# Kernel tuning notes

Measured on AMD Instinct MI355X. Metric: run time of the kernel, lower is better.

The kernel has to match this reference:

```python
import jax, jax.numpy as jnp
import numpy as np

N, C, H, W = 8, 192, 112, 112
TEMPERATURE = 0.1


def setup_inputs() -> dict:
    key = jax.random.key(0)
    k1, k2 = jax.random.split(key)
    features = jax.random.normal(k1, (N, C, H, W), dtype=jnp.float32)
    # Raw per-pixel directions in {-1, 0, 1}; clip the neighbor coordinate into
    # bounds and recompute the direction so EVERY neighbor is valid. The torch
    # module's broadcasting (labels[:, i, j] vs an (N, M) gather) only works when
    # all N neighbors are valid at each pixel, so this matches its assumptions.
    raw = jax.random.randint(k2, (N, 2, H, W), -1, 2)
    ii = jnp.arange(H)[None, :, None]
    jj = jnp.arange(W)[None, None, :]
    d0 = jnp.clip(ii + raw[:, 0], 0, H - 1) - ii
    d1 = jnp.clip(jj + raw[:, 1], 0, W - 1) - jj
    directions = jnp.stack([d0, d1], axis=1).astype(jnp.int32)
    # Single-class labels: the original loss is -inf whenever any mask entry is 0
    # (log of exactly 0), so a finite, comparable baseline needs matching labels.
    labels = jnp.zeros((N, H, W), dtype=jnp.int32)
    return {"features": features, "labels": labels, "directions": directions}


def reference(features, labels, directions):
    # F.normalize(features, dim=1): x / max(||x||_2, eps)
    norm = jnp.linalg.norm(features, axis=1, keepdims=True)
    fn = features / jnp.maximum(norm, 1e-12)

    ii = jnp.arange(H)[None, :, None]
    jj = jnp.arange(W)[None, None, :]
    ni = ii + directions[:, 0]  # (N, H, W), in-bounds by construction
    nj = jj + directions[:, 1]  # (N, H, W)

    # Torch: features[:, :, neighbor_i, neighbor_j] gathers the M(==N) neighbor
    # coordinates across ALL batch elements -> (N, C, N, H, W) = [n, c, m, i, j]
    gathered = fn[:, :, ni, nj]
    # logits[n, m, i, j] = <fn[n, :, i, j], fn[n, :, ni[m,i,j], nj[m,i,j]]> / T
    logits = jnp.einsum('ncij,ncmij->nmij', fn, gathered) / TEMPERATURE

    # mask[n, m, i, j] = (labels[m, i, j] == labels[n, ni[m,i,j], nj[m,i,j]])
    # (torch broadcasts labels[:, i, j] along the first axis of the (N, M) gather)
    labels_g = labels[:, ni, nj]  # (N, N, H, W) = [n, m, i, j]
    mask = (labels[None, :, :, :] == labels_g).astype(fn.dtype)

    exp_l = jnp.exp(logits) * mask
    denom = jnp.sum(exp_l, axis=1, keepdims=True)  # sum over m
    # sum_{i,j} mean_{n,m}(.) / (H*W) == global mean over (n, m, i, j)
    loss = (-jnp.log(exp_l / (denom + 1e-6))).mean()
    return loss
```

## Files before the change

kernel.cpp:

```cpp
#include <hip/hip_runtime.h>
#include <math.h>


namespace {
constexpr int N_ = 8, C_ = 192, H_ = 112, W_ = 112;
constexpr int HW = H_ * W_;
constexpr int TPY = 8, TPX = 16;
constexpr int RS = 19;
constexpr int SLOTE = 192;
constexpr int NT = 128;
constexpr int CW = C_ / 2;
constexpr int KCH = 8;
constexpr int GRP = KCH / 2;
constexpr int NCHUNK = CW / KCH;
constexpr int GX = W_ / TPX, GY = H_ / TPY;
constexpr int NBLK = GX * GY * N_;
constexpr float INV_T = 10.0f;
constexpr double TOTAL = (double)N_ * N_ * H_ * W_;
}

__device__ __forceinline__ float sel3(int d, float a, float b, float c) {
    float r = (d < 0) ? a : b;
    return (d > 0) ? c : r;
}

__device__ __forceinline__ float px_loss(
    const float l[3][3], int gi, int gj, int n,
    const int* __restrict__ labels, const int* __restrict__ dirs)
{
    const int pix = gi * W_ + gj;
    float denom = 0.f, sumlog = 0.f;
#pragma unroll
    for (int m = 0; m < N_; ++m) {
        int d0 = dirs[((m * 2 + 0) * H_ + gi) * W_ + gj];
        int d1 = dirs[((m * 2 + 1) * H_ + gi) * W_ + gj];
        float r0 = sel3(d1, l[0][0], l[0][1], l[0][2]);
        float r1 = sel3(d1, l[1][0], l[1][1], l[1][2]);
        float r2 = sel3(d1, l[2][0], l[2][1], l[2][2]);
        float lm = sel3(d0, r0, r1, r2);
        int labm = labels[m * HW + pix];
        int labn = labels[n * HW + (gi + d0) * W_ + (gj + d1)];
        bool msk = (labm == labn);
        float e = msk ? __expf(lm) : 0.f;
        denom += e;
        sumlog += msk ? lm : -INFINITY;
    }
    return 8.0f * __logf(denom + 1e-6f) - sumlog;
}

extern "C" __global__ void __launch_bounds__(NT, 2)
dcl_main(const float* __restrict__ feat,
         const int* __restrict__ labels,
         const int* __restrict__ dirs,
         double* __restrict__ partial, int use_partial)
{
    __shared__ float2 tl[2 * 2 * GRP * SLOTE];
    __shared__ float  ssb[SLOTE];
    __shared__ float2 exch[64 * 9];

    const int tid = threadIdx.x, lane = tid & 63, wv = tid >> 6;
    const int gx0 = blockIdx.x * TPX, gy0 = blockIdx.y * TPY, n = blockIdx.z;

    int g0, g1, g2;
    {
        int s = lane, r = s / RS, c = s - r * RS;
        g0 = min(max(gy0 + r - 1, 0), H_ - 1) * W_ + min(max(gx0 + c - 1, 0), W_ - 1);
        s = lane + 64; r = s / RS; c = s - r * RS;
        g1 = min(max(gy0 + r - 1, 0), H_ - 1) * W_ + min(max(gx0 + c - 1, 0), W_ - 1);
        s = lane + 128; r = s / RS; c = s - r * RS;
        g2 = min(max(gy0 + r - 1, 0), H_ - 1) * W_ + min(max(gx0 + c - 1, 0), W_ - 1);
    }
    const int py = lane >> 3, pxp = lane & 7;
    const int wb = py * RS + 2 * pxp;
    const float* __restrict__ plane =
        feat + ((size_t)n * C_ + (size_t)wv * CW) * HW;

#define TLP(buf, g) (tl + (((wv * 2 + (buf)) * GRP + (g)) * SLOTE))

    float sA[9], sB[9];
    #pragma unroll
    for (int k = 0; k < 9; ++k) { sA[k] = 0.f; sB[k] = 0.f; }
    float ss0 = 0.f, ss1 = 0.f, ss2 = 0.f;

    {
        float v[24];
        #pragma unroll
        for (int k = 0; k < KCH; ++k) {
            v[k]      = plane[(size_t)k * HW + g0];
            v[8 + k]  = plane[(size_t)k * HW + g1];
            v[16 + k] = plane[(size_t)k * HW + g2];
        }
        #pragma unroll
        for (int g = 0; g < GRP; ++g) {
            TLP(0, g)[lane]       = make_float2(v[2 * g],      v[2 * g + 1]);
            TLP(0, g)[lane + 64]  = make_float2(v[8 + 2 * g],  v[8 + 2 * g + 1]);
            TLP(0, g)[lane + 128] = make_float2(v[16 + 2 * g], v[16 + 2 * g + 1]);
        }
        #pragma unroll
        for (int k = 0; k < KCH; ++k) {
            ss0 = fmaf(v[k], v[k], ss0);
            ss1 = fmaf(v[8 + k], v[8 + k], ss1);
            ss2 = fmaf(v[16 + k], v[16 + k], ss2);
        }
    }

    for (int t = 0; t < NCHUNK; ++t) {
        float v[24];
        const bool more = (t + 1 < NCHUNK);
        if (more) {
            const float* p = plane + (size_t)(t + 1) * KCH * HW;
            #pragma unroll
            for (int k = 0; k < KCH; ++k) {
                v[k]      = p[(size_t)k * HW + g0];
                v[8 + k]  = p[(size_t)k * HW + g1];
                v[16 + k] = p[(size_t)k * HW + g2];
            }
        }
        const int buf = t & 1;
        #pragma unroll
        for (int g = 0; g < GRP; ++g) {
            const float2* __restrict__ cp = TLP(buf, g);
            float2 w00 = cp[wb],          w01 = cp[wb + 1],          w02 = cp[wb + 2],          w03 = cp[wb + 3];
            float2 w10 = cp[wb + RS],     w11 = cp[wb + RS + 1],     w12 = cp[wb + RS + 2],     w13 = cp[wb + RS + 3];
            float2 w20 = cp[wb + 2 * RS], w21 = cp[wb + 2 * RS + 1], w22 = cp[wb + 2 * RS + 2], w23 = cp[wb + 2 * RS + 3];
            const float2 fA = w11, fB = w12;
            sA[0] = fmaf(fA.x, w00.x, fmaf(fA.y, w00.y, sA[0]));
            sA[1] = fmaf(fA.x, w01.x, fmaf(fA.y, w01.y, sA[1]));
            sA[2] = fmaf(fA.x, w02.x, fmaf(fA.y, w02.y, sA[2]));
            sA[3] = fmaf(fA.x, w10.x, fmaf(fA.y, w10.y, sA[3]));
            sA[4] = fmaf(fA.x, w11.x, fmaf(fA.y, w11.y, sA[4]));
            sA[5] = fmaf(fA.x, w12.x, fmaf(fA.y, w12.y, sA[5]));
            sA[6] = fmaf(fA.x, w20.x, fmaf(fA.y, w20.y, sA[6]));
            sA[7] = fmaf(fA.x, w21.x, fmaf(fA.y, w21.y, sA[7]));
            sA[8] = fmaf(fA.x, w22.x, fmaf(fA.y, w22.y, sA[8]));
            sB[0] = fmaf(fB.x, w01.x, fmaf(fB.y, w01.y, sB[0]));
            sB[1] = fmaf(fB.x, w02.x, fmaf(fB.y, w02.y, sB[1]));
            sB[2] = fmaf(fB.x, w03.x, fmaf(fB.y, w03.y, sB[2]));
            sB[3] = fmaf(fB.x, w11.x, fmaf(fB.y, w11.y, sB[3]));
            sB[4] = fmaf(fB.x, w12.x, fmaf(fB.y, w12.y, sB[4]));
            sB[5] = fmaf(fB.x, w13.x, fmaf(fB.y, w13.y, sB[5]));
            sB[6] = fmaf(fB.x, w21.x, fmaf(fB.y, w21.y, sB[6]));
            sB[7] = fmaf(fB.x, w22.x, fmaf(fB.y, w22.y, sB[7]));
            sB[8] = fmaf(fB.x, w23.x, fmaf(fB.y, w23.y, sB[8]));
        }
        if (more) {
            const int nb = buf ^ 1;
            #pragma unroll
            for (int g = 0; g < GRP; ++g) {
                TLP(nb, g)[lane]       = make_float2(v[2 * g],      v[2 * g + 1]);
                TLP(nb, g)[lane + 64]  = make_float2(v[8 + 2 * g],  v[8 + 2 * g + 1]);
                TLP(nb, g)[lane + 128] = make_float2(v[16 + 2 * g], v[16 + 2 * g + 1]);
            }
            #pragma unroll
            for (int k = 0; k < KCH; ++k) {
                ss0 = fmaf(v[k], v[k], ss0);
                ss1 = fmaf(v[8 + k], v[8 + k], ss1);
                ss2 = fmaf(v[16 + k], v[16 + k], ss2);
            }
        }
    }

    if (wv == 1) {
        #pragma unroll
        for (int k = 0; k < 9; ++k) exch[lane * 9 + k] = make_float2(sA[k], sB[k]);
        ssb[lane] = ss0; ssb[lane + 64] = ss1; ssb[lane + 128] = ss2;
    }
    __syncthreads();
    if (wv == 0) {
        ssb[lane]       = 1.0f / fmaxf(sqrtf(ss0 + ssb[lane]), 1e-12f);
        ssb[lane + 64]  = 1.0f / fmaxf(sqrtf(ss1 + ssb[lane + 64]), 1e-12f);
        ssb[lane + 128] = 1.0f / fmaxf(sqrtf(ss2 + ssb[lane + 128]), 1e-12f);
    }
    __syncthreads();

    if (wv == 0) {
        #pragma unroll
        for (int k = 0; k < 9; ++k) {
            float2 e = exch[lane * 9 + k];
            sA[k] += e.x; sB[k] += e.y;
        }
        float iv[3][4];
        #pragma unroll
        for (int r = 0; r < 3; ++r)
            #pragma unroll
            for (int c = 0; c < 4; ++c)
                iv[r][c] = ssb[wb + r * RS + c];
        const float iA = iv[1][1] * INV_T, iB = iv[1][2] * INV_T;
        float lA[3][3], lB[3][3];
        #pragma unroll
        for (int r = 0; r < 3; ++r)
            #pragma unroll
            for (int c = 0; c < 3; ++c) {
                lA[r][c] = sA[r * 3 + c] * iA * iv[r][c];
                lB[r][c] = sB[r * 3 + c] * iB * iv[r][c + 1];
            }
        const int gi = gy0 + py, gj = gx0 + 2 * pxp;
        float lp = px_loss(lA, gi, gj, n, labels, dirs)
                 + px_loss(lB, gi, gj + 1, n, labels, dirs);
        #pragma unroll
        for (int off = 32; off > 0; off >>= 1) lp += __shfl_down(lp, off, 64);
        if (lane == 0) {
            const int bid = (blockIdx.z * gridDim.y + blockIdx.y) * gridDim.x + blockIdx.x;
            if (use_partial) partial[bid] = (double)lp;
            else atomicAdd(partial, (double)lp);
        }
    }
#undef TLP
}

extern "C" __global__ void __launch_bounds__(256)
dcl_final(const double* __restrict__ partial, float* __restrict__ out, int nblk)
{
    const int tid = threadIdx.x;
    double s = 0.0;
    for (int i = tid; i < nblk; i += 256) s += partial[i];
    #pragma unroll
    for (int off = 32; off > 0; off >>= 1) s += __shfl_down(s, off, 64);
    __shared__ double red[4];
    const int lane = tid & 63, wv = tid >> 6;
    if (lane == 0) red[wv] = s;
    __syncthreads();
    if (tid == 0) out[0] = (float)((red[0] + red[1] + red[2] + red[3]) / TOTAL);
}

extern "C" void kernel_launch(void* const* d_in, const int* in_sizes, int n_in,
                              void* d_out, int out_size, void* d_ws, size_t ws_size,
                              hipStream_t stream) {
    const float* feat   = (const float*)d_in[0];
    const int*   labels = (const int*)d_in[1];
    const int*   dirs   = (const int*)d_in[2];
    double* acc = (double*)d_ws;
    float*  out = (float*)d_out;

    const int use_partial = (ws_size >= (size_t)NBLK * sizeof(double)) ? 1 : 0;
    if (!use_partial) hipMemsetAsync(acc, 0, sizeof(double), stream);
    dim3 grid(GX, GY, N_);
    dcl_main<<<grid, NT, 0, stream>>>(feat, labels, dirs, acc, use_partial);
    dcl_final<<<1, 256, 0, stream>>>(acc, out, use_partial ? NBLK : 1);
}
```

Measured before the change: 143.7 us.

## Retile to 2x56 strips with single-wave blocks over all channels

Replaces the 8x16 tile split across two waves, each handling half the channels, with a 2-row by 56-column tile handled by one 64-thread wave over all 192 channels. This drops the cross-wave exchange of partial dot products and norms and lowers the halo overhead per pixel. LDS reads become float4 vector loads. The trade-offs: only 56 of 64 lanes do compute, a barrier runs after every chunk, and the 58-element row stride may not keep the float4 LDS reads 16-byte aligned.

Result: faster. 130.9 us (-8.9%).

```diff
diff --git a/kernel.cpp b/kernel.cpp
--- a/kernel.cpp
+++ b/kernel.cpp
@@ -5,15 +5,18 @@
 namespace {
 constexpr int N_ = 8, C_ = 192, H_ = 112, W_ = 112;
 constexpr int HW = H_ * W_;
-constexpr int TPY = 8, TPX = 16;
-constexpr int RS = 19;
-constexpr int SLOTE = 192;
-constexpr int NT = 128;
-constexpr int CW = C_ / 2;
+constexpr int TH = 2;
+constexpr int WSX = 56;
+constexpr int TROWS = TH + 2;
+constexpr int RS = WSX + 2;
+constexpr int TILE_E = TROWS * RS;
+constexpr int NT = 64;
+constexpr int NS4 = TILE_E - 3 * NT;
+constexpr int NPAIR = TH * (WSX / 2);
 constexpr int KCH = 8;
 constexpr int GRP = KCH / 2;
-constexpr int NCHUNK = CW / KCH;
-constexpr int GX = W_ / TPX, GY = H_ / TPY;
+constexpr int NCHUNK = C_ / KCH;
+constexpr int GX = W_ / WSX, GY = H_ / TH;
 constexpr int NBLK = GX * GY * N_;
 constexpr float INV_T = 10.0f;
 constexpr double TOTAL = (double)N_ * N_ * H_ * W_;
@@ -48,137 +51,157 @@
     return 8.0f * __logf(denom + 1e-6f) - sumlog;
 }
 
-extern "C" __global__ void __launch_bounds__(NT, 2)
+extern "C" __global__ void __launch_bounds__(NT, 4)
 dcl_main(const float* __restrict__ feat,
          const int* __restrict__ labels,
          const int* __restrict__ dirs,
          double* __restrict__ partial, int use_partial)
 {
-    __shared__ float2 tl[2 * 2 * GRP * SLOTE];
-    __shared__ float  ssb[SLOTE];
-    __shared__ float2 exch[64 * 9];
-
-    const int tid = threadIdx.x, lane = tid & 63, wv = tid >> 6;
-    const int gx0 = blockIdx.x * TPX, gy0 = blockIdx.y * TPY, n = blockIdx.z;
-
-    int g0, g1, g2;
+    alignas(16) __shared__ float2 tl[2 * GRP * TILE_E];
+    __shared__ float ssb[TILE_E];
+
+    const int lane = threadIdx.x;
+    const int gx0 = blockIdx.x * WSX;
+    const int gy0 = blockIdx.y * TH;
+    const int n   = blockIdx.z;
+
+    const bool has4 = (lane < NS4);
+    int gofs[4];
+    #pragma unroll
+    for (int sI = 0; sI < 4; ++sI) {
+        int s = lane + sI * NT;
+        if (s >= TILE_E) s = TILE_E - 1;
+        int r = s / RS, c = s - r * RS;
+        gofs[sI] = min(max(gy0 + r - 1, 0), H_ - 1) * W_
+                 + min(max(gx0 + c - 1, 0), W_ - 1);
+    }
+
+    const bool is_px = (lane < NPAIR);
+    const int py  = lane / (WSX / 2);
+    const int pxp = lane - py * (WSX / 2);
+    const int wb  = py * RS + 2 * pxp;
+
+    const float* __restrict__ plane = feat + (size_t)n * C_ * HW;
+
+#define TLP(buf, g) (tl + ((buf) * GRP + (g)) * TILE_E)
+
+    float sA[9], sB[9];
+    #pragma unroll
+    for (int k = 0; k < 9; ++k) { sA[k] = 0.f; sB[k] = 0.f; }
+    float ss[4] = {0.f, 0.f, 0.f, 0.f};
+
     {
-        int s = lane, r = s / RS, c = s - r * RS;
-        g0 = min(max(gy0 + r - 1, 0), H_ - 1) * W_ + min(max(gx0 + c - 1, 0), W_ - 1);
-        s = lane + 64; r = s / RS; c = s - r * RS;
-        g1 = min(max(gy0 + r - 1, 0), H_ - 1) * W_ + min(max(gx0 + c - 1, 0), W_ - 1);
-        s = lane + 128; r = s / RS; c = s - r * RS;
-        g2 = min(max(gy0 + r - 1, 0), H_ - 1) * W_ + min(max(gx0 + c - 1, 0), W_ - 1);
-    }
-    const int py = lane >> 3, pxp = lane & 7;
-    const int wb = py * RS + 2 * pxp;
-    const float* __restrict__ plane =
-        feat + ((size_t)n * C_ + (size_t)wv * CW) * HW;
-
-#define TLP(buf, g) (tl + (((wv * 2 + (buf)) * GRP + (g)) * SLOTE))
-
-    float sA[9], sB[9];
-    #pragma unroll
-    for (int k = 0; k < 9; ++k) { sA[k] = 0.f; sB[k] = 0.f; }
-    float ss0 = 0.f, ss1 = 0.f, ss2 = 0.f;
-
-    {
-        float v[24];
+        float v[4][KCH];
         #pragma unroll
         for (int k = 0; k < KCH; ++k) {
-            v[k]      = plane[(size_t)k * HW + g0];
-            v[8 + k]  = plane[(size_t)k * HW + g1];
-            v[16 + k] = plane[(size_t)k * HW + g2];
-        }
+            v[0][k] = plane[(size_t)k * HW + gofs[0]];
+            v[1][k] = plane[(size_t)k * HW + gofs[1]];
+            v[2][k] = plane[(size_t)k * HW + gofs[2]];
+        }
+        if (has4)
+            #pragma unroll
+            for (int k = 0; k < KCH; ++k) v[3][k] = plane[(size_t)k * HW + gofs[3]];
         #pragma unroll
         for (int g = 0; g < GRP; ++g) {
-            TLP(0, g)[lane]       = make_float2(v[2 * g],      v[2 * g + 1]);
-            TLP(0, g)[lane + 64]  = make_float2(v[8 + 2 * g],  v[8 + 2 * g + 1]);
-            TLP(0, g)[lane + 128] = make_float2(v[16 + 2 * g], v[16 + 2 * g + 1]);
-        }
+            TLP(0, g)[lane]            = make_float2(v[0][2*g], v[0][2*g+1]);
+            TLP(0, g)[lane + NT]       = make_float2(v[1][2*g], v[1][2*g+1]);
+            TLP(0, g)[lane + 2 * NT]   = make_float2(v[2][2*g], v[2][2*g+1]);
+        }
+        if (has4)
+            #pragma unroll
+            for (int g = 0; g < GRP; ++g)
+                TLP(0, g)[lane + 3 * NT] = make_float2(v[3][2*g], v[3][2*g+1]);
         #pragma unroll
         for (int k = 0; k < KCH; ++k) {
-            ss0 = fmaf(v[k], v[k], ss0);
-            ss1 = fmaf(v[8 + k], v[8 + k], ss1);
-            ss2 = fmaf(v[16 + k], v[16 + k], ss2);
-        }
-    }
+            ss[0] = fmaf(v[0][k], v[0][k], ss[0]);
+            ss[1] = fmaf(v[1][k], v[1][k], ss[1]);
+            ss[2] = fmaf(v[2][k], v[2][k], ss[2]);
+            if (has4) ss[3] = fmaf(v[3][k], v[3][k], ss[3]);
+        }
+    }
+    __syncthreads();
 
     for (int t = 0; t < NCHUNK; ++t) {
-        float v[24];
+        float v[4][KCH];
         const bool more = (t + 1 < NCHUNK);
         if (more) {
             const float* p = plane + (size_t)(t + 1) * KCH * HW;
             #pragma unroll
             for (int k = 0; k < KCH; ++k) {
-                v[k]      = p[(size_t)k * HW + g0];
-                v[8 + k]  = p[(size_t)k * HW + g1];
-                v[16 + k] = p[(size_t)k * HW + g2];
-            }
-        }
+                v[0][k] = p[(size_t)k * HW + gofs[0]];
+                v[1][k] = p[(size_t)k * HW + gofs[1]];
+                v[2][k] = p[(size_t)k * HW + gofs[2]];
+            }
+            if (has4)
+                #pragma unroll
+                for (int k = 0; k < KCH; ++k) v[3][k] = p[(size_t)k * HW + gofs[3]];
+        }
+
         const int buf = t & 1;
-        #pragma unroll
-        for (int g = 0; g < GRP; ++g) {
-            const float2* __restrict__ cp = TLP(buf, g);
-            float2 w00 = cp[wb],          w01 = cp[wb + 1],          w02 = cp[wb + 2],          w03 = cp[wb + 3];
-            float2 w10 = cp[wb + RS],     w11 = cp[wb + RS + 1],     w12 = cp[wb + RS + 2],     w13 = cp[wb + RS + 3];
-            float2 w20 = cp[wb + 2 * RS], w21 = cp[wb + 2 * RS + 1], w22 = cp[wb + 2 * RS + 2], w23 = cp[wb + 2 * RS + 3];
-            const float2 fA = w11, fB = w12;
-            sA[0] = fmaf(fA.x, w00.x, fmaf(fA.y, w00.y, sA[0]));
-            sA[1] = fmaf(fA.x, w01.x, fmaf(fA.y, w01.y, sA[1]));
-            sA[2] = fmaf(fA.x, w02.x, fmaf(fA.y, w02.y, sA[2]));
-            sA[3] = fmaf(fA.x, w10.x, fmaf(fA.y, w10.y, sA[3]));
-            sA[4] = fmaf(fA.x, w11.x, fmaf(fA.y, w11.y, sA[4]));
-            sA[5] = fmaf(fA.x, w12.x, fmaf(fA.y, w12.y, sA[5]));
-            sA[6] = fmaf(fA.x, w20.x, fmaf(fA.y, w20.y, sA[6]));
-            sA[7] = fmaf(fA.x, w21.x, fmaf(fA.y, w21.y, sA[7]));
-            sA[8] = fmaf(fA.x, w22.x, fmaf(fA.y, w22.y, sA[8]));
-            sB[0] = fmaf(fB.x, w01.x, fmaf(fB.y, w01.y, sB[0]));
-            sB[1] = fmaf(fB.x, w02.x, fmaf(fB.y, w02.y, sB[1]));
-            sB[2] = fmaf(fB.x, w03.x, fmaf(fB.y, w03.y, sB[2]));
-            sB[3] = fmaf(fB.x, w11.x, fmaf(fB.y, w11.y, sB[3]));
-            sB[4] = fmaf(fB.x, w12.x, fmaf(fB.y, w12.y, sB[4]));
-            sB[5] = fmaf(fB.x, w13.x, fmaf(fB.y, w13.y, sB[5]));
-            sB[6] = fmaf(fB.x, w21.x, fmaf(fB.y, w21.y, sB[6]));
-            sB[7] = fmaf(fB.x, w22.x, fmaf(fB.y, w22.y, sB[7]));
-            sB[8] = fmaf(fB.x, w23.x, fmaf(fB.y, w23.y, sB[8]));
-        }
+        if (is_px) {
+            #pragma unroll
+            for (int g = 0; g < GRP; ++g) {
+                const float2* __restrict__ cp = TLP(buf, g);
+                float4 L0 = *reinterpret_cast<const float4*>(cp + wb);
+                float4 R0 = *reinterpret_cast<const float4*>(cp + wb + 2);
+                float4 L1 = *reinterpret_cast<const float4*>(cp + wb + RS);
+                float4 R1 = *reinterpret_cast<const float4*>(cp + wb + RS + 2);
+                float4 L2 = *reinterpret_cast<const float4*>(cp + wb + 2 * RS);
+                float4 R2 = *reinterpret_cast<const float4*>(cp + wb + 2 * RS + 2);
+                const float fAx = L1.z, fAy = L1.w;
+                const float fBx = R1.x, fBy = R1.y;
+                sA[0] = fmaf(fAx, L0.x, fmaf(fAy, L0.y, sA[0]));
+                sA[1] = fmaf(fAx, L0.z, fmaf(fAy, L0.w, sA[1]));
+                sA[2] = fmaf(fAx, R0.x, fmaf(fAy, R0.y, sA[2]));
+                sA[3] = fmaf(fAx, L1.x, fmaf(fAy, L1.y, sA[3]));
+                sA[4] = fmaf(fAx, L1.z, fmaf(fAy, L1.w, sA[4]));
+                sA[5] = fmaf(fAx, R1.x, fmaf(fAy, R1.y, sA[5]));
+                sA[6] = fmaf(fAx, L2.x, fmaf(fAy, L2.y, sA[6]));
+                sA[7] = fmaf(fAx, L2.z, fmaf(fAy, L2.w, sA[7]));
+                sA[8] = fmaf(fAx, R2.x, fmaf(fAy, R2.y, sA[8]));
+                sB[0] = fmaf(fBx, L0.z, fmaf(fBy, L0.w, sB[0]));
+                sB[1] = fmaf(fBx, R0.x, fmaf(fBy, R0.y, sB[1]));
+                sB[2] = fmaf(fBx, R0.z, fmaf(fBy, R0.w, sB[2]));
+                sB[3] = fmaf(fBx, L1.z, fmaf(fBy, L1.w, sB[3]));
+                sB[4] = fmaf(fBx, R1.x, fmaf(fBy, R1.y, sB[4]));
+                sB[5] = fmaf(fBx, R1.z, fmaf(fBy, R1.w, sB[5]));
+                sB[6] = fmaf(fBx, L2.z, fmaf(fBy, L2.w, sB[6]));
+                sB[7] = fmaf(fBx, R2.x, fmaf(fBy, R2.y, sB[7]));
+                sB[8] = fmaf(fBx, R2.z, fmaf(fBy, R2.w, sB[8]));
+            }
+        }
+
         if (more) {
             const int nb = buf ^ 1;
             #pragma unroll
             for (int g = 0; g < GRP; ++g) {
-                TLP(nb, g)[lane]       = make_float2(v[2 * g],      v[2 * g + 1]);
-                TLP(nb, g)[lane + 64]  = make_float2(v[8 + 2 * g],  v[8 + 2 * g + 1]);
-                TLP(nb, g)[lane + 128] = make_float2(v[16 + 2 * g], v[16 + 2 * g + 1]);
-            }
+                TLP(nb, g)[lane]          = make_float2(v[0][2*g], v[0][2*g+1]);
+                TLP(nb, g)[lane + NT]     = make_float2(v[1][2*g], v[1][2*g+1]);
+                TLP(nb, g)[lane + 2 * NT] = make_float2(v[2][2*g], v[2][2*g+1]);
+            }
+            if (has4)
+                #pragma unroll
+                for (int g = 0; g < GRP; ++g)
+                    TLP(nb, g)[lane + 3 * NT] = make_float2(v[3][2*g], v[3][2*g+1]);
             #pragma unroll
             for (int k = 0; k < KCH; ++k) {
-                ss0 = fmaf(v[k], v[k], ss0);
-                ss1 = fmaf(v[8 + k], v[8 + k], ss1);
-                ss2 = fmaf(v[16 + k], v[16 + k], ss2);
-            }
-        }
-    }
-
-    if (wv == 1) {
-        #pragma unroll
-        for (int k = 0; k < 9; ++k) exch[lane * 9 + k] = make_float2(sA[k], sB[k]);
-        ssb[lane] = ss0; ssb[lane + 64] = ss1; ssb[lane + 128] = ss2;
-    }
+                ss[0] = fmaf(v[0][k], v[0][k], ss[0]);
+                ss[1] = fmaf(v[1][k], v[1][k], ss[1]);
+                ss[2] = fmaf(v[2][k], v[2][k], ss[2]);
+                if (has4) ss[3] = fmaf(v[3][k], v[3][k], ss[3]);
+            }
+        }
+        __syncthreads();
+    }
+
+    ssb[lane]          = 1.0f / fmaxf(sqrtf(ss[0]), 1e-12f);
+    ssb[lane + NT]     = 1.0f / fmaxf(sqrtf(ss[1]), 1e-12f);
+    ssb[lane + 2 * NT] = 1.0f / fmaxf(sqrtf(ss[2]), 1e-12f);
+    if (has4) ssb[lane + 3 * NT] = 1.0f / fmaxf(sqrtf(ss[3]), 1e-12f);
     __syncthreads();
-    if (wv == 0) {
-        ssb[lane]       = 1.0f / fmaxf(sqrtf(ss0 + ssb[lane]), 1e-12f);
-        ssb[lane + 64]  = 1.0f / fmaxf(sqrtf(ss1 + ssb[lane + 64]), 1e-12f);
-        ssb[lane + 128] = 1.0f / fmaxf(sqrtf(ss2 + ssb[lane + 128]), 1e-12f);
-    }
-    __syncthreads();
-
-    if (wv == 0) {
-        #pragma unroll
-        for (int k = 0; k < 9; ++k) {
-            float2 e = exch[lane * 9 + k];
-            sA[k] += e.x; sB[k] += e.y;
-        }
+
+    float lp = 0.0f;
+    if (is_px) {
         float iv[3][4];
         #pragma unroll
         for (int r = 0; r < 3; ++r)
@@ -195,15 +218,15 @@
                 lB[r][c] = sB[r * 3 + c] * iB * iv[r][c + 1];
             }
         const int gi = gy0 + py, gj = gx0 + 2 * pxp;
-        float lp = px_loss(lA, gi, gj, n, labels, dirs)
-                 + px_loss(lB, gi, gj + 1, n, labels, dirs);
-        #pragma unroll
-        for (int off = 32; off > 0; off >>= 1) lp += __shfl_down(lp, off, 64);
-        if (lane == 0) {
-            const int bid = (blockIdx.z * gridDim.y + blockIdx.y) * gridDim.x + blockIdx.x;
-            if (use_partial) partial[bid] = (double)lp;
-            else atomicAdd(partial, (double)lp);
-        }
+        lp = px_loss(lA, gi, gj, n, labels, dirs)
+           + px_loss(lB, gi, gj + 1, n, labels, dirs);
+    }
+    #pragma unroll
+    for (int off = 32; off > 0; off >>= 1) lp += __shfl_down(lp, off, 64);
+    if (lane == 0) {
+        const int bid = (blockIdx.z * gridDim.y + blockIdx.y) * gridDim.x + blockIdx.x;
+        if (use_partial) partial[bid] = (double)lp;
+        else atomicAdd(partial, (double)lp);
     }
 #undef TLP
 }
```
